# Kernel optimization log

Hardware: AMD Instinct MI355X
Metric: run time of the kernel (lower is better)

The kernel has to match this reference:

```python
import jax, jax.numpy as jnp
import numpy as np

STRIDE = 4
EPS = 1e-6  # torch.pairwise_distance default eps


def setup_inputs() -> dict:
    key = jax.random.key(0)
    k1, k2 = jax.random.split(key)
    a = jax.random.normal(k1, (4, 256, 256, 256), dtype=jnp.float32)
    b = jax.random.normal(k2, (4, 256, 256, 256), dtype=jnp.float32)
    return {"a": a, "b": b}


def _patches(x, stride):
    # nn.Unfold(1, stride): sample every stride-th pixel -> [B, N, C]
    B, C, H, W = x.shape
    xp = x[:, :, ::stride, ::stride]            # [B, C, h, w]
    h, w = xp.shape[2], xp.shape[3]
    return xp.reshape(B, C, h * w).transpose(0, 2, 1), h, w


def reference(a, b):
    B, C, H, W = a.shape
    av, h, w = _patches(a, STRIDE)              # [B, N, C]
    bv, _, _ = _patches(b, STRIDE)              # [B, M, C]
    a2 = jnp.sum(av * av, axis=-1)              # [B, N]
    b2 = jnp.sum(bv * bv, axis=-1)              # [B, M]
    ab = jnp.einsum('bnc,bmc->bnm', av, bv)     # [B, N, M]
    sa = jnp.sum(av, axis=-1)
    sb = jnp.sum(bv, axis=-1)
    d2 = (a2[:, :, None] + b2[:, None, :] - 2.0 * ab
          + 2.0 * EPS * (sa[:, :, None] - sb[:, None, :]) + C * EPS * EPS)
    d2min = jnp.min(d2, axis=-1)                # sqrt is monotone -> min of d2 first
    l2 = jnp.sqrt(jnp.maximum(d2min, 0.0))      # [B, N]
    scores = 2.0 * jax.nn.sigmoid(-l2)
    sm = scores.reshape(B, h, w)
    # F.interpolate(..., mode='nearest') with integer scale == pixel repeat
    out = jnp.repeat(jnp.repeat(sm, STRIDE, axis=1), STRIDE, axis=2)
    return out[:, None, :, :]                   # [B, 1, H, W]
```

## Files before the change

kernel.cpp:

```cpp
#include <hip/hip_runtime.h>
#include <math.h>


#define BATCH 4
#define CH    256
#define HH    256
#define WW    256
#define NPTS  4096
#define EPSV  1e-6f

typedef _Float16 half8 __attribute__((ext_vector_type(8)));
typedef float    f32x4 __attribute__((ext_vector_type(4)));

typedef __attribute__((address_space(1))) const void global_cvoid;
typedef __attribute__((address_space(3))) void lds_void;

#define AC_OFF   0u
#define BC_OFF   (8u << 20)
#define A2_OFF   (16u << 20)
#define B2_OFF   ((16u << 20) + (64u << 10))
#define DP_OFF   ((16u << 20) + (128u << 10))
#define WS_TOTAL ((16u << 20) + (384u << 10))

__global__ __launch_bounds__(256) void gm_gather(
    const float* __restrict__ srcA, const float* __restrict__ srcB,
    unsigned char* __restrict__ ws)
{
  const int t  = threadIdx.x;
  const int h  = blockIdx.x;
  const int b  = blockIdx.y;
  const int z  = blockIdx.z;
  const int w  = t & 63;
  const int wv = t >> 6;

  const float* src = z ? srcB : srcA;
  unsigned char* dst = ws + (z ? BC_OFF : AC_OFF);
  float* norms = (float*)(ws + (z ? B2_OFF : A2_OFF));
  const float epsSign = z ? -2.0f * EPSV : 2.0f * EPSV;
  const float addC    = z ? (float)CH * EPSV * EPSV : 0.0f;

  const float* rowbase = src + ((size_t)b * CH) * (HH * WW)
                             + (size_t)(h * 4) * WW + (size_t)(w * 4);
  float ssum = 0.0f, ssq = 0.0f;
  #pragma unroll
  for (int i = 0; i < 8; ++i) {
    const int kc = wv * 8 + i;
    half8 hv;
    #pragma unroll
    for (int j = 0; j < 8; ++j) {
      const int c = kc * 8 + j;
      float v = rowbase[(size_t)c * (HH * WW)];
      ssum += v;
      ssq  = fmaf(v, v, ssq);
      hv[j] = (_Float16)v;
    }
    *reinterpret_cast<half8*>(dst + ((size_t)((b * 32 + kc) * NPTS + h * 64 + w)) * 16) = hv;
  }

  __shared__ float red[2][4][64];
  red[0][wv][w] = ssum;
  red[1][wv][w] = ssq;
  __syncthreads();
  if (t < 64) {
    float sm = red[0][0][t] + red[0][1][t] + red[0][2][t] + red[0][3][t];
    float sq = red[1][0][t] + red[1][1][t] + red[1][2][t] + red[1][3][t];
    norms[b * NPTS + h * 64 + t] = fmaf(epsSign, sm, sq) + addC;
  }
}

__device__ __forceinline__ void stage_b_tile(const unsigned char* __restrict__ Bc,
                                             int b, int mbase,
                                             unsigned char* dst, int t, int wv) {
  #pragma unroll
  for (int r = 0; r < 4; ++r) {
    unsigned x  = (unsigned)(r * 512 + t) * 16;
    unsigned lb = x ^ (((x >> 9) & 7) << 4);
    unsigned m_l = lb >> 9;
    unsigned kcb = (lb & 511) >> 4;
    const unsigned char* srcp =
        Bc + ((size_t)((b * 32 + kcb) * NPTS + mbase + m_l)) * 16;
    __builtin_amdgcn_global_load_lds((global_cvoid*)srcp,
                                     (lds_void*)(dst + (r * 8192 + wv * 1024)),
                                     16, 0, 0);
  }
}

__global__ __launch_bounds__(512, 2) void gm_gemm_min(
    const unsigned char* __restrict__ Ac, const unsigned char* __restrict__ Bc,
    const float* __restrict__ a2p, const float* __restrict__ b2pc,
    float* __restrict__ d2part)
{
  __shared__ __align__(16) unsigned char smem[65536];

  const int t  = threadIdx.x;
  const int l  = t & 63;
  const int wv = t >> 6;
  const int q  = (l >> 4) & 3;

  const int orig    = blockIdx.x;
  const int logical = (orig & 7) * 32 + (orig >> 3);
  const int ns = logical & 15;
  const int mq = (logical >> 4) & 3;
  const int b  = logical >> 6;
  const int nbase  = ns * 256;
  const int mstart = mq * 1024;

  half8 af[2][8];
  #pragma unroll
  for (int half = 0; half < 2; ++half) {
    #pragma unroll
    for (int r = 0; r < 8; ++r) {
      unsigned x  = (unsigned)(r * 512 + t) * 16;
      unsigned lb = x ^ (((x >> 9) & 7) << 4);
      unsigned n_l = lb >> 9;
      unsigned kcb = (lb & 511) >> 4;
      const unsigned char* srcp =
          Ac + ((size_t)((b * 32 + kcb) * NPTS + nbase + half * 128 + n_l)) * 16;
      __builtin_amdgcn_global_load_lds((global_cvoid*)srcp,
                                       (lds_void*)(smem + (r * 8192 + wv * 1024)),
                                       16, 0, 0);
    }
    asm volatile("s_waitcnt vmcnt(0)" ::: "memory");
    __builtin_amdgcn_s_barrier();
    if ((wv >> 2) == half) {
      #pragma unroll
      for (int nf = 0; nf < 2; ++nf) {
        const unsigned rr   = (wv & 3) * 32 + nf * 16 + (l & 15);
        const unsigned base = rr * 512 + q * 16;
        const unsigned sw   = (rr & 7) << 4;
        #pragma unroll
        for (int kk = 0; kk < 8; ++kk)
          af[nf][kk] = *reinterpret_cast<const half8*>(smem + ((base + kk * 64) ^ sw));
      }
    }
    asm volatile("s_waitcnt lgkmcnt(0)" ::: "memory");
    __builtin_amdgcn_s_barrier();
  }

  float rmin[2][4];
  #pragma unroll
  for (int nf = 0; nf < 2; ++nf)
    #pragma unroll
    for (int r = 0; r < 4; ++r) rmin[nf][r] = 3.0e38f;

  stage_b_tile(Bc, b, mstart, smem, t, wv);
  for (int mt = 0; mt < 16; ++mt) {
    unsigned char* cb = (mt & 1) ? smem + 32768 : smem;
    unsigned char* nb = (mt & 1) ? smem : smem + 32768;
    if (mt < 15) {
      stage_b_tile(Bc, b, mstart + (mt + 1) * 64, nb, t, wv);
      asm volatile("s_waitcnt vmcnt(4)" ::: "memory");
    } else {
      asm volatile("s_waitcnt vmcnt(0)" ::: "memory");
    }
    __builtin_amdgcn_s_barrier();

    f32x4 acc[2][4];
    #pragma unroll
    for (int nf = 0; nf < 2; ++nf)
      #pragma unroll
      for (int ms = 0; ms < 4; ++ms) acc[nf][ms] = (f32x4){0.f, 0.f, 0.f, 0.f};

    #pragma unroll
    for (int kk = 0; kk < 8; ++kk) {
      half8 bf[4];
      #pragma unroll
      for (int ms = 0; ms < 4; ++ms) {
        const unsigned rr   = ms * 16 + (l & 15);
        const unsigned addr = (rr * 512 + kk * 64 + q * 16) ^ ((rr & 7) << 4);
        bf[ms] = *reinterpret_cast<const half8*>(cb + addr);
      }
      #pragma unroll
      for (int ms = 0; ms < 4; ++ms) {
        acc[0][ms] = __builtin_amdgcn_mfma_f32_16x16x32_f16(af[0][kk], bf[ms], acc[0][ms], 0, 0, 0);
        acc[1][ms] = __builtin_amdgcn_mfma_f32_16x16x32_f16(af[1][kk], bf[ms], acc[1][ms], 0, 0, 0);
      }
    }

    const int mbase = mstart + mt * 64;
    #pragma unroll
    for (int ms = 0; ms < 4; ++ms) {
      const float bp = b2pc[b * NPTS + mbase + ms * 16 + (l & 15)];
      #pragma unroll
      for (int r = 0; r < 4; ++r) {
        rmin[0][r] = fminf(rmin[0][r], fmaf(-2.0f, acc[0][ms][r], bp));
        rmin[1][r] = fminf(rmin[1][r], fmaf(-2.0f, acc[1][ms][r], bp));
      }
    }
    __builtin_amdgcn_s_barrier();
  }

  #pragma unroll
  for (int nf = 0; nf < 2; ++nf)
    #pragma unroll
    for (int r = 0; r < 4; ++r) {
      float v = rmin[nf][r];
      v = fminf(v, __shfl_xor(v, 1, 64));
      v = fminf(v, __shfl_xor(v, 2, 64));
      v = fminf(v, __shfl_xor(v, 4, 64));
      v = fminf(v, __shfl_xor(v, 8, 64));
      if ((l & 15) == 0) {
        const int n = nbase + wv * 32 + nf * 16 + q * 4 + r;
        d2part[(size_t)(b * NPTS + n) * 4 + mq] = v + a2p[b * NPTS + n];
      }
    }
}

__global__ __launch_bounds__(256) void gm_finalize(
    const float* __restrict__ d2part, float* __restrict__ out)
{
  const int id = blockIdx.x * 256 + threadIdx.x;
  const f32x4 v4 = *reinterpret_cast<const f32x4*>(d2part + (size_t)id * 4);
  const float d2 = fminf(fminf(v4[0], v4[1]), fminf(v4[2], v4[3]));
  const float l2 = sqrtf(fmaxf(d2, 0.0f));
  const float s  = 2.0f / (1.0f + expf(l2));
  const int b = id >> 12;
  const int n = id & 4095;
  const int h = n >> 6, w = n & 63;
  float4 v = make_float4(s, s, s, s);
  float* obase = out + ((size_t)(b * 256 + h * 4)) * 256 + w * 4;
  #pragma unroll
  for (int i = 0; i < 4; ++i)
    *reinterpret_cast<float4*>(obase + (size_t)i * 256) = v;
}

__global__ void gm_sentinel(float* out) { out[0] = 1.0e6f; }

extern "C" void kernel_launch(void* const* d_in, const int* in_sizes, int n_in,
                              void* d_out, int out_size, void* d_ws, size_t ws_size,
                              hipStream_t stream) {
  const float* a = (const float*)d_in[0];
  const float* b = (const float*)d_in[1];
  float* out = (float*)d_out;
  unsigned char* ws = (unsigned char*)d_ws;

  if (ws_size < (size_t)WS_TOTAL) {
    gm_sentinel<<<1, 1, 0, stream>>>(out);
    return;
  }

  gm_gather<<<dim3(64, 4, 2), 256, 0, stream>>>(a, b, ws);
  gm_gemm_min<<<256, 512, 0, stream>>>(
      ws + AC_OFF, ws + BC_OFF,
      (const float*)(ws + A2_OFF), (const float*)(ws + B2_OFF),
      (float*)(ws + DP_OFF));
  gm_finalize<<<64, 256, 0, stream>>>((const float*)(ws + DP_OFF), out);
}
```

Before: 69.10 us.

## Switch GEMM-min to 32x32x16 MFMA with 128-row B tiles and 2D wave split

Replaces the 16x16x32 MFMA tiling with 32x32x16 MFMAs. Each wave now owns 64 A rows and 64 B columns per tile, using a 4x2 wave grid with 128-column B tiles double-buffered in 128KB of LDS. The whole 256-row A block is staged at once, and per-wave partial minima go into an 8-way partial buffer that the finalize kernel reduces. This aims to cut LDS reads per MFMA and raise matrix-core efficiency. The cost is more registers (rmin/acc of 16 each, af[2][16]) and higher LDS use, which may limit occupancy below the declared 2 blocks per CU.

```diff
diff --git a/kernel.cpp b/kernel.cpp
--- a/kernel.cpp
+++ b/kernel.cpp
@@ -9,8 +9,9 @@
 #define NPTS  4096
 #define EPSV  1e-6f
 
-typedef _Float16 half8 __attribute__((ext_vector_type(8)));
-typedef float    f32x4 __attribute__((ext_vector_type(4)));
+typedef _Float16 half8  __attribute__((ext_vector_type(8)));
+typedef float    f32x4  __attribute__((ext_vector_type(4)));
+typedef float    f32x16 __attribute__((ext_vector_type(16)));
 
 typedef __attribute__((address_space(1))) const void global_cvoid;
 typedef __attribute__((address_space(3))) void lds_void;
@@ -20,7 +21,7 @@
 #define A2_OFF   (16u << 20)
 #define B2_OFF   ((16u << 20) + (64u << 10))
 #define DP_OFF   ((16u << 20) + (128u << 10))
-#define WS_TOTAL ((16u << 20) + (384u << 10))
+#define WS_TOTAL ((16u << 20) + (640u << 10))
 
 __global__ __launch_bounds__(256) void gm_gather(
     const float* __restrict__ srcA, const float* __restrict__ srcB,
@@ -70,9 +71,10 @@
 
 __device__ __forceinline__ void stage_b_tile(const unsigned char* __restrict__ Bc,
                                              int b, int mbase,
-                                             unsigned char* dst, int t, int wv) {
-  #pragma unroll
-  for (int r = 0; r < 4; ++r) {
+                                             unsigned char* dst, int t) {
+  const int wv = t >> 6;
+  #pragma unroll
+  for (int r = 0; r < 8; ++r) {
     unsigned x  = (unsigned)(r * 512 + t) * 16;
     unsigned lb = x ^ (((x >> 9) & 7) << 4);
     unsigned m_l = lb >> 9;
@@ -90,12 +92,15 @@
     const float* __restrict__ a2p, const float* __restrict__ b2pc,
     float* __restrict__ d2part)
 {
-  __shared__ __align__(16) unsigned char smem[65536];
+  __shared__ __align__(16) unsigned char smem[131072];
 
   const int t  = threadIdx.x;
   const int l  = t & 63;
   const int wv = t >> 6;
-  const int q  = (l >> 4) & 3;
+  const int wn = wv & 3;
+  const int wm = wv >> 2;
+  const int ln31  = l & 31;
+  const int khalf = l >> 5;
 
   const int orig    = blockIdx.x;
   const int logical = (orig & 7) * 32 + (orig >> 3);
@@ -105,87 +110,74 @@
   const int nbase  = ns * 256;
   const int mstart = mq * 1024;
 
-  half8 af[2][8];
-  #pragma unroll
-  for (int half = 0; half < 2; ++half) {
-    #pragma unroll
-    for (int r = 0; r < 8; ++r) {
-      unsigned x  = (unsigned)(r * 512 + t) * 16;
-      unsigned lb = x ^ (((x >> 9) & 7) << 4);
-      unsigned n_l = lb >> 9;
-      unsigned kcb = (lb & 511) >> 4;
-      const unsigned char* srcp =
-          Ac + ((size_t)((b * 32 + kcb) * NPTS + nbase + half * 128 + n_l)) * 16;
-      __builtin_amdgcn_global_load_lds((global_cvoid*)srcp,
-                                       (lds_void*)(smem + (r * 8192 + wv * 1024)),
-                                       16, 0, 0);
-    }
-    asm volatile("s_waitcnt vmcnt(0)" ::: "memory");
-    __builtin_amdgcn_s_barrier();
-    if ((wv >> 2) == half) {
-      #pragma unroll
-      for (int nf = 0; nf < 2; ++nf) {
-        const unsigned rr   = (wv & 3) * 32 + nf * 16 + (l & 15);
-        const unsigned base = rr * 512 + q * 16;
-        const unsigned sw   = (rr & 7) << 4;
-        #pragma unroll
-        for (int kk = 0; kk < 8; ++kk)
-          af[nf][kk] = *reinterpret_cast<const half8*>(smem + ((base + kk * 64) ^ sw));
-      }
-    }
-    asm volatile("s_waitcnt lgkmcnt(0)" ::: "memory");
-    __builtin_amdgcn_s_barrier();
-  }
-
-  float rmin[2][4];
+  #pragma unroll
+  for (int r = 0; r < 16; ++r) {
+    unsigned x  = (unsigned)(r * 512 + t) * 16;
+    unsigned lb = x ^ (((x >> 9) & 7) << 4);
+    unsigned n_l = lb >> 9;
+    unsigned kcb = (lb & 511) >> 4;
+    const unsigned char* srcp =
+        Ac + ((size_t)((b * 32 + kcb) * NPTS + nbase + n_l)) * 16;
+    __builtin_amdgcn_global_load_lds((global_cvoid*)srcp,
+                                     (lds_void*)(smem + (r * 8192 + wv * 1024)),
+                                     16, 0, 0);
+  }
+  asm volatile("s_waitcnt vmcnt(0)" ::: "memory");
+  __builtin_amdgcn_s_barrier();
+
+  half8 af[2][16];
+  #pragma unroll
+  for (int nf = 0; nf < 2; ++nf) {
+    const unsigned rr = wn * 64 + nf * 32 + ln31;
+    const unsigned sw = (rr & 7) << 4;
+    #pragma unroll
+    for (int kk = 0; kk < 16; ++kk)
+      af[nf][kk] = *reinterpret_cast<const half8*>(
+          smem + ((rr * 512 + khalf * 16 + kk * 32) ^ sw));
+  }
+  asm volatile("s_waitcnt lgkmcnt(0)" ::: "memory");
+  __builtin_amdgcn_s_barrier();
+
+  float rmin[2][16];
   #pragma unroll
   for (int nf = 0; nf < 2; ++nf)
     #pragma unroll
-    for (int r = 0; r < 4; ++r) rmin[nf][r] = 3.0e38f;
-
-  stage_b_tile(Bc, b, mstart, smem, t, wv);
-  for (int mt = 0; mt < 16; ++mt) {
-    unsigned char* cb = (mt & 1) ? smem + 32768 : smem;
-    unsigned char* nb = (mt & 1) ? smem : smem + 32768;
-    if (mt < 15) {
-      stage_b_tile(Bc, b, mstart + (mt + 1) * 64, nb, t, wv);
-      asm volatile("s_waitcnt vmcnt(4)" ::: "memory");
+    for (int r = 0; r < 16; ++r) rmin[nf][r] = 3.0e38f;
+
+  stage_b_tile(Bc, b, mstart, smem, t);
+  for (int mt = 0; mt < 8; ++mt) {
+    unsigned char* cb = (mt & 1) ? smem + 65536 : smem;
+    unsigned char* nb = (mt & 1) ? smem : smem + 65536;
+    if (mt < 7) {
+      stage_b_tile(Bc, b, mstart + (mt + 1) * 128, nb, t);
+      asm volatile("s_waitcnt vmcnt(8)" ::: "memory");
     } else {
       asm volatile("s_waitcnt vmcnt(0)" ::: "memory");
     }
     __builtin_amdgcn_s_barrier();
 
-    f32x4 acc[2][4];
-    #pragma unroll
-    for (int nf = 0; nf < 2; ++nf)
+    const int mbase = mstart + mt * 128;
+    #pragma unroll
+    for (int ms = 0; ms < 2; ++ms) {
+      const unsigned rrB = wm * 64 + ms * 32 + ln31;
+      const unsigned swB = (rrB & 7) << 4;
+
+      f32x16 acc0 = (f32x16)(0.0f);
+      f32x16 acc1 = (f32x16)(0.0f);
       #pragma unroll
-      for (int ms = 0; ms < 4; ++ms) acc[nf][ms] = (f32x4){0.f, 0.f, 0.f, 0.f};
-
-    #pragma unroll
-    for (int kk = 0; kk < 8; ++kk) {
-      half8 bf[4];
+      for (int kk = 0; kk < 16; ++kk) {
+        const half8 bf = *reinterpret_cast<const half8*>(
+            cb + ((rrB * 512 + khalf * 16 + kk * 32) ^ swB));
+        acc0 = __builtin_amdgcn_mfma_f32_32x32x16_f16(af[0][kk], bf, acc0, 0, 0, 0);
+        acc1 = __builtin_amdgcn_mfma_f32_32x32x16_f16(af[1][kk], bf, acc1, 0, 0, 0);
+      }
+
+      const float bp = b2pc[b * NPTS + mbase + wm * 64 + ms * 32 + ln31];
       #pragma unroll
-      for (int ms = 0; ms < 4; ++ms) {
-        const unsigned rr   = ms * 16 + (l & 15);
-        const unsigned addr = (rr * 512 + kk * 64 + q * 16) ^ ((rr & 7) << 4);
-        bf[ms] = *reinterpret_cast<const half8*>(cb + addr);
+      for (int r = 0; r < 16; ++r) {
+        rmin[0][r] = fminf(rmin[0][r], fmaf(-2.0f, acc0[r], bp));
+        rmin[1][r] = fminf(rmin[1][r], fmaf(-2.0f, acc1[r], bp));
       }
-      #pragma unroll
-      for (int ms = 0; ms < 4; ++ms) {
-        acc[0][ms] = __builtin_amdgcn_mfma_f32_16x16x32_f16(af[0][kk], bf[ms], acc[0][ms], 0, 0, 0);
-        acc[1][ms] = __builtin_amdgcn_mfma_f32_16x16x32_f16(af[1][kk], bf[ms], acc[1][ms], 0, 0, 0);
-      }
-    }
-
-    const int mbase = mstart + mt * 64;
-    #pragma unroll
-    for (int ms = 0; ms < 4; ++ms) {
-      const float bp = b2pc[b * NPTS + mbase + ms * 16 + (l & 15)];
-      #pragma unroll
-      for (int r = 0; r < 4; ++r) {
-        rmin[0][r] = fminf(rmin[0][r], fmaf(-2.0f, acc[0][ms][r], bp));
-        rmin[1][r] = fminf(rmin[1][r], fmaf(-2.0f, acc[1][ms][r], bp));
-      }
     }
     __builtin_amdgcn_s_barrier();
   }
@@ -193,15 +185,16 @@
   #pragma unroll
   for (int nf = 0; nf < 2; ++nf)
     #pragma unroll
-    for (int r = 0; r < 4; ++r) {
+    for (int r = 0; r < 16; ++r) {
       float v = rmin[nf][r];
       v = fminf(v, __shfl_xor(v, 1, 64));
       v = fminf(v, __shfl_xor(v, 2, 64));
       v = fminf(v, __shfl_xor(v, 4, 64));
       v = fminf(v, __shfl_xor(v, 8, 64));
-      if ((l & 15) == 0) {
-        const int n = nbase + wv * 32 + nf * 16 + q * 4 + r;
-        d2part[(size_t)(b * NPTS + n) * 4 + mq] = v + a2p[b * NPTS + n];
+      v = fminf(v, __shfl_xor(v, 16, 64));
+      if (ln31 == 0) {
+        const int n = nbase + wn * 64 + nf * 32 + (r & 3) + 8 * (r >> 2) + 4 * khalf;
+        d2part[(size_t)(b * NPTS + n) * 8 + mq * 2 + wm] = v + a2p[b * NPTS + n];
       }
     }
 }
@@ -210,8 +203,10 @@
     const float* __restrict__ d2part, float* __restrict__ out)
 {
   const int id = blockIdx.x * 256 + threadIdx.x;
-  const f32x4 v4 = *reinterpret_cast<const f32x4*>(d2part + (size_t)id * 4);
-  const float d2 = fminf(fminf(v4[0], v4[1]), fminf(v4[2], v4[3]));
+  const f32x4 u = *reinterpret_cast<const f32x4*>(d2part + (size_t)id * 8);
+  const f32x4 w4 = *reinterpret_cast<const f32x4*>(d2part + (size_t)id * 8 + 4);
+  float d2 = fminf(fminf(fminf(u[0], u[1]), fminf(u[2], u[3])),
+                   fminf(fminf(w4[0], w4[1]), fminf(w4[2], w4[3])));
   const float l2 = sqrtf(fmaxf(d2, 0.0f));
   const float s  = 2.0f / (1.0f + expf(l2));
   const int b = id >> 12;
```

New measurement: 86.18 us. +24.7%, slower.
